# Optimization experiments

Hardware: AMD Instinct MI355X
Metric: run time of the kernel (lower is better)

The kernel has to match this reference:

```python
import jax, jax.numpy as jnp
import numpy as np

N_NODES = 100000


def sage_conv(x, src, dst, w_self, w_neigh, b):
    # DGL SAGEConv('mean'): h = x @ W_self + mean_{u in N(v)} x_u @ W_neigh + b
    ones = jnp.ones(src.shape[0], dtype=x.dtype)
    deg = jax.ops.segment_sum(ones, dst, num_segments=N_NODES)  # [N]
    neigh_sum = jax.ops.segment_sum(x[src], dst, num_segments=N_NODES)  # [N, F]
    neigh = neigh_sum / jnp.clip(deg, 1.0)[:, None]  # isolated nodes -> 0
    return x @ w_self + neigh @ w_neigh + b


def setup_inputs() -> dict:
    key = jax.random.key(0)
    ks = jax.random.split(key, 9)
    nfeat, nhid, nclass = 128, 128, 2
    E = 1600000
    x = jax.random.normal(ks[0], (N_NODES, nfeat), dtype=jnp.float32)
    src = jax.random.randint(ks[1], (E,), 0, N_NODES)
    dst = jax.random.randint(ks[2], (E,), 0, N_NODES)
    s1 = 1.0 / np.sqrt(nfeat)
    s2 = 1.0 / np.sqrt(nhid)
    return {
        "x": x,
        "src": src,
        "dst": dst,
        "w_self1": jax.random.uniform(ks[3], (nfeat, nhid), jnp.float32, -s1, s1),
        "w_neigh1": jax.random.uniform(ks[4], (nfeat, nhid), jnp.float32, -s1, s1),
        "b1": jnp.zeros((nhid,), jnp.float32),
        "w_self2": jax.random.uniform(ks[5], (nhid, nclass), jnp.float32, -s2, s2),
        "w_neigh2": jax.random.uniform(ks[6], (nhid, nclass), jnp.float32, -s2, s2),
        "b2": jnp.zeros((nclass,), jnp.float32),
    }


def reference(x, src, dst, w_self1, w_neigh1, b1, w_self2, w_neigh2, b2):
    h = jax.nn.relu(sage_conv(x, src, dst, w_self1, w_neigh1, b1))
    h = sage_conv(h, src, dst, w_self2, w_neigh2, b2)
    return jax.nn.log_softmax(h, axis=1)
```

## Files before the change

kernel.cpp:

```cpp
#include <hip/hip_runtime.h>
#include <hip/hip_bf16.h>


#define N_FEAT 128
#define CSHIFT 9
#define CNODES 512
#define NBINS 256
#define CCAP 9728
#define BATCH 8192
#define EPT 32
#define BF_BLOCKS 256
#define PW_BLOCKS 128

typedef __attribute__((ext_vector_type(8))) short short8;
typedef __attribute__((ext_vector_type(8))) unsigned short ushort8_t;
typedef __attribute__((ext_vector_type(16))) float f32x16;

__device__ __forceinline__ float bf16_bits_to_f32(ushort u) {
    union { unsigned int i; float f; } c;
    c.i = ((unsigned int)u) << 16;
    return c.f;
}
__device__ __forceinline__ ushort f32_to_bf16_bits(float f) {
    return __bfloat16_as_ushort(__float2bfloat16(f));
}

__global__ __launch_bounds__(256) void prep_and_split_kernel(
    const int* __restrict__ src, const int* __restrict__ dst,
    int* __restrict__ ccursor, unsigned* __restrict__ cbuf, int E,
    const float* __restrict__ x, ushort* __restrict__ xb, int n4,
    const float* __restrict__ w1, const float* __restrict__ w2,
    ushort* __restrict__ wt, int nms) {
    __shared__ unsigned stage[BATCH];
    __shared__ int cntw[4][NBINS];
    __shared__ int curw[4][NBINS];
    __shared__ int excl[NBINS];
    __shared__ int incl[NBINS];
    __shared__ int gpos[NBINS];
    __shared__ int wsum[4];
    int tid = threadIdx.x;
    int bid = blockIdx.x;

    if (bid >= nms) {
        int rb = bid - nms;
        if (rb < BF_BLOCKS) {
            int i = rb * 256 + tid;
            int stride = BF_BLOCKS * 256;
            for (; i < n4; i += stride) {
                float4 v = ((const float4*)x)[i];
                ushort4 r;
                r.x = f32_to_bf16_bits(v.x);
                r.y = f32_to_bf16_bits(v.y);
                r.z = f32_to_bf16_bits(v.z);
                r.w = f32_to_bf16_bits(v.w);
                ((ushort4*)xb)[i] = r;
            }
        } else {
            int id = (rb - BF_BLOCKS) * 256 + tid;
            int nn = id >> 8;
            int k = id & 255;
            float v = (k < 128) ? w1[k * 128 + nn] : w2[(k - 128) * 128 + nn];
            wt[nn * 256 + k] = f32_to_bf16_bits(v);
        }
        return;
    }

    int wv = tid >> 6;
    int lane = tid & 63;
    int base = bid * BATCH;
    int total = min(BATCH, E - base);

    unsigned pk[EPT];
    int bn[EPT];
    for (int i = tid; i < 4 * NBINS; i += 256) ((int*)cntw)[i] = 0;
    __syncthreads();
    #pragma unroll
    for (int k = 0; k < EPT; ++k) {
        int e = base + k * 256 + tid;
        if (e < E) {
            int d = dst[e];
            int sv = src[e];
            bn[k] = d >> CSHIFT;
            pk[k] = ((unsigned)(d & (CNODES - 1)) << 17) | (unsigned)sv;
            atomicAdd(&cntw[wv][bn[k]], 1);
        } else {
            bn[k] = -1;
        }
    }
    __syncthreads();
    int c0 = cntw[0][tid], c1 = cntw[1][tid], c2 = cntw[2][tid], c3 = cntw[3][tid];
    cntw[0][tid] = 0;
    cntw[1][tid] = c0;
    cntw[2][tid] = c0 + c1;
    cntw[3][tid] = c0 + c1 + c2;
    int c = c0 + c1 + c2 + c3;
    int val = c;
    #pragma unroll
    for (int off = 1; off < 64; off <<= 1) {
        int t = __shfl_up(val, off);
        if (lane >= off) val += t;
    }
    if (lane == 63) wsum[wv] = val;
    __syncthreads();
    #pragma unroll
    for (int i = 0; i < 4; ++i)
        if (i < wv) val += wsum[i];
    incl[tid] = val;
    int e0 = val - c;
    excl[tid] = e0;
    curw[0][tid] = e0 + cntw[0][tid];
    curw[1][tid] = e0 + cntw[1][tid];
    curw[2][tid] = e0 + cntw[2][tid];
    curw[3][tid] = e0 + cntw[3][tid];
    gpos[tid] = (c > 0) ? atomicAdd(&ccursor[tid], c) : 0;
    __syncthreads();
    #pragma unroll
    for (int k = 0; k < EPT; ++k) {
        if (bn[k] >= 0) {
            int ofs = atomicAdd(&curw[wv][bn[k]], 1);
            stage[ofs] = pk[k];
        }
    }
    __syncthreads();
    for (int i = tid; i < total; i += 256) {
        int lo = 0, hi = NBINS - 1;
        while (lo < hi) {
            int mid = (lo + hi) >> 1;
            if (incl[mid] > i) hi = mid; else lo = mid + 1;
        }
        int b = lo;
        int target = gpos[b] + (i - excl[b]);
        cbuf[(size_t)b * CCAP + target] = stage[i];
    }
}

__global__ __launch_bounds__(512) void build_csr2_kernel(
    const unsigned* __restrict__ cbuf, const int* __restrict__ ccnt,
    int* __restrict__ row_ptr, int* __restrict__ csr, int N, int E) {
    __shared__ int hist[CNODES];
    __shared__ int cur[CNODES];
    __shared__ int wred[8];
    __shared__ int cstart_s;
    int cb = blockIdx.x;
    int tid = threadIdx.x;
    int lane = tid & 63;
    int w = tid >> 6;

    int v = (tid < cb) ? ccnt[tid] : 0;
    #pragma unroll
    for (int off = 32; off > 0; off >>= 1) v += __shfl_xor(v, off);
    if (lane == 0) wred[w] = v;
    hist[tid] = 0;
    __syncthreads();
    if (tid == 0) {
        int t = 0;
        #pragma unroll
        for (int i = 0; i < 8; ++i) t += wred[i];
        cstart_s = t;
    }
    if (cb == 0 && tid == 0) row_ptr[N] = E;
    int cnt = ccnt[cb];
    size_t bbase = (size_t)cb * CCAP;
    __syncthreads();
    int base = cstart_s;

    for (int e = tid; e < cnt; e += 512) {
        unsigned p = cbuf[bbase + e];
        atomicAdd(&hist[p >> 17], 1);
    }
    __syncthreads();
    int c = hist[tid];
    int val = c;
    #pragma unroll
    for (int off = 1; off < 64; off <<= 1) {
        int t = __shfl_up(val, off);
        if (lane >= off) val += t;
    }
    if (lane == 63) wred[w] = val;
    __syncthreads();
    #pragma unroll
    for (int i = 0; i < 8; ++i)
        if (i < w) val += wred[i];
    int excl = val - c;
    int node = cb * CNODES + tid;
    if (node < N) row_ptr[node] = base + excl;
    cur[tid] = excl;
    __syncthreads();
    for (int e = tid; e < cnt; e += 512) {
        unsigned p = cbuf[bbase + e];
        int bin = p >> 17;
        int ofs = atomicAdd(&cur[bin], 1);
        csr[base + ofs] = (int)(p & 0x1FFFF);
    }
}

__global__ __launch_bounds__(256) void aggregate_bf16_kernel(
    const ushort* __restrict__ xb, const int* __restrict__ row_ptr,
    const int* __restrict__ csr, ushort* __restrict__ out, int n) {
    int v = blockIdx.x * 4 + (threadIdx.x >> 6);
    int lane = threadIdx.x & 63;
    int sub = lane >> 4;
    int fc = lane & 15;
    if (v >= n) return;
    int beg = row_ptr[v];
    int end = row_ptr[v + 1];
    float acc[8];
    #pragma unroll
    for (int j = 0; j < 8; ++j) acc[j] = 0.f;
    const ushort* xfc = xb + fc * 8;
    int e = beg;
    for (; e + 16 <= end; e += 16) {
        int s0 = csr[e + sub];
        int s1 = csr[e + 4 + sub];
        int s2 = csr[e + 8 + sub];
        int s3 = csr[e + 12 + sub];
        ushort8_t t0 = *(const ushort8_t*)(xfc + (size_t)s0 * N_FEAT);
        ushort8_t t1 = *(const ushort8_t*)(xfc + (size_t)s1 * N_FEAT);
        ushort8_t t2 = *(const ushort8_t*)(xfc + (size_t)s2 * N_FEAT);
        ushort8_t t3 = *(const ushort8_t*)(xfc + (size_t)s3 * N_FEAT);
        #pragma unroll
        for (int j = 0; j < 8; ++j) acc[j] += bf16_bits_to_f32(t0[j]);
        #pragma unroll
        for (int j = 0; j < 8; ++j) acc[j] += bf16_bits_to_f32(t1[j]);
        #pragma unroll
        for (int j = 0; j < 8; ++j) acc[j] += bf16_bits_to_f32(t2[j]);
        #pragma unroll
        for (int j = 0; j < 8; ++j) acc[j] += bf16_bits_to_f32(t3[j]);
    }
    if (e + 8 <= end) {
        int s0 = csr[e + sub];
        int s1 = csr[e + 4 + sub];
        ushort8_t t0 = *(const ushort8_t*)(xfc + (size_t)s0 * N_FEAT);
        ushort8_t t1 = *(const ushort8_t*)(xfc + (size_t)s1 * N_FEAT);
        #pragma unroll
        for (int j = 0; j < 8; ++j) acc[j] += bf16_bits_to_f32(t0[j]);
        #pragma unroll
        for (int j = 0; j < 8; ++j) acc[j] += bf16_bits_to_f32(t1[j]);
        e += 8;
    }
    if (e + 4 <= end) {
        int s0 = csr[e + sub];
        ushort8_t t0 = *(const ushort8_t*)(xfc + (size_t)s0 * N_FEAT);
        #pragma unroll
        for (int j = 0; j < 8; ++j) acc[j] += bf16_bits_to_f32(t0[j]);
        e += 4;
    }
    int rem = end - e;
    if (sub < rem) {
        int s0 = csr[e + sub];
        ushort8_t t0 = *(const ushort8_t*)(xfc + (size_t)s0 * N_FEAT);
        #pragma unroll
        for (int j = 0; j < 8; ++j) acc[j] += bf16_bits_to_f32(t0[j]);
    }
    #pragma unroll
    for (int j = 0; j < 8; ++j) {
        acc[j] += __shfl_xor(acc[j], 16);
        acc[j] += __shfl_xor(acc[j], 32);
    }
    if (lane < 16) {
        int deg = end - beg;
        float inv = (deg > 0) ? 1.0f / (float)deg : 0.0f;
        ushort8_t r;
        #pragma unroll
        for (int j = 0; j < 8; ++j)
            r[j] = f32_to_bf16_bits(acc[j] * inv);
        *(ushort8_t*)(out + (size_t)v * N_FEAT + lane * 8) = r;
    }
}

__global__ __launch_bounds__(256) void gemm1_fused_kernel(
    const ushort* __restrict__ xb, const ushort* __restrict__ nbb,
    const ushort* __restrict__ wt, const float* __restrict__ b,
    const float* __restrict__ ws2, const float* __restrict__ wn2,
    float* __restrict__ s_out, float* __restrict__ z_out, int n) {
    __shared__ ushort As[128 * 72];
    __shared__ ushort Bs[128 * 72];
    int tid = threadIdx.x;
    int wave = tid >> 6;
    int lane = tid & 63;
    int m = lane & 31;
    int half = lane >> 5;
    int block_row = blockIdx.x * 128;

    f32x16 acc[4];
    #pragma unroll
    for (int t = 0; t < 4; ++t)
        #pragma unroll
        for (int i = 0; i < 16; ++i) acc[t][i] = 0.0f;

    for (int kc = 0; kc < 4; ++kc) {
        const ushort* A = (kc < 2) ? xb : nbb;
        int k0 = (kc & 1) * 64;
        #pragma unroll
        for (int l = 0; l < 4; ++l) {
            int idx = l * 256 + tid;
            int r = idx >> 3;
            int p = idx & 7;
            int node = block_row + r;
            ushort8_t v;
            if (node < n) {
                v = *(const ushort8_t*)(A + (size_t)node * N_FEAT + k0 + p * 8);
            } else {
                #pragma unroll
                for (int q = 0; q < 8; ++q) v[q] = 0;
            }
            *(ushort8_t*)(&As[r * 72 + p * 8]) = v;
        }
        #pragma unroll
        for (int l = 0; l < 4; ++l) {
            int idx = l * 256 + tid;
            int cc = idx >> 3;
            int p = idx & 7;
            ushort8_t v = *(const ushort8_t*)(wt + (size_t)cc * 256 + kc * 64 + p * 8);
            *(ushort8_t*)(&Bs[cc * 72 + p * 8]) = v;
        }
        __syncthreads();
        #pragma unroll
        for (int ks = 0; ks < 4; ++ks) {
            int koff = ks * 16 + half * 8;
            short8 a = *(const short8*)(&As[(32 * wave + m) * 72 + koff]);
            short8 bf0 = *(const short8*)(&Bs[(0 * 32 + m) * 72 + koff]);
            short8 bf1 = *(const short8*)(&Bs[(1 * 32 + m) * 72 + koff]);
            short8 bf2 = *(const short8*)(&Bs[(2 * 32 + m) * 72 + koff]);
            short8 bf3 = *(const short8*)(&Bs[(3 * 32 + m) * 72 + koff]);
            acc[0] = __builtin_amdgcn_mfma_f32_32x32x16_bf16(a, bf0, acc[0], 0, 0, 0);
            acc[1] = __builtin_amdgcn_mfma_f32_32x32x16_bf16(a, bf1, acc[1], 0, 0, 0);
            acc[2] = __builtin_amdgcn_mfma_f32_32x32x16_bf16(a, bf2, acc[2], 0, 0, 0);
            acc[3] = __builtin_amdgcn_mfma_f32_32x32x16_bf16(a, bf3, acc[3], 0, 0, 0);
        }
        __syncthreads();
    }

    float bcol[4], wsc[4][2], wnc[4][2];
    #pragma unroll
    for (int t = 0; t < 4; ++t) {
        int col = t * 32 + m;
        bcol[t] = b[col];
        float2 a = ((const float2*)ws2)[col];
        float2 q = ((const float2*)wn2)[col];
        wsc[t][0] = a.x; wsc[t][1] = a.y;
        wnc[t][0] = q.x; wnc[t][1] = q.y;
    }
    #pragma unroll
    for (int reg = 0; reg < 16; ++reg) {
        int rowin = (reg & 3) + 8 * (reg >> 2) + 4 * half;
        int node = block_row + 32 * wave + rowin;
        float p0 = 0.f, p1 = 0.f, q0 = 0.f, q1 = 0.f;
        #pragma unroll
        for (int t = 0; t < 4; ++t) {
            float hv = fmaxf(acc[t][reg] + bcol[t], 0.0f);
            p0 += hv * wsc[t][0]; p1 += hv * wsc[t][1];
            q0 += hv * wnc[t][0]; q1 += hv * wnc[t][1];
        }
        #pragma unroll
        for (int off = 1; off < 32; off <<= 1) {
            p0 += __shfl_xor(p0, off);
            p1 += __shfl_xor(p1, off);
            q0 += __shfl_xor(q0, off);
            q1 += __shfl_xor(q1, off);
        }
        if (m == 0 && node < n) {
            ((float2*)s_out)[node] = make_float2(p0, p1);
            ((float2*)z_out)[node] = make_float2(q0, q1);
        }
    }
}

__global__ __launch_bounds__(256) void layer2b_kernel(
    const float* __restrict__ s_in, const float* __restrict__ z,
    const int* __restrict__ row_ptr, const int* __restrict__ csr,
    const float* __restrict__ b, float* __restrict__ out, int n) {
    int v = blockIdx.x * 16 + (threadIdx.x >> 4);
    int sl = threadIdx.x & 15;
    if (v >= n) return;
    int beg = row_ptr[v];
    int end = row_ptr[v + 1];
    float a0 = 0.f, a1 = 0.f;
    for (int e = beg + sl; e < end; e += 16) {
        float2 t = ((const float2*)z)[csr[e]];
        a0 += t.x; a1 += t.y;
    }
    #pragma unroll
    for (int off = 8; off > 0; off >>= 1) {
        a0 += __shfl_xor(a0, off);
        a1 += __shfl_xor(a1, off);
    }
    if (sl == 0) {
        int deg = end - beg;
        float inv = (deg > 0) ? 1.0f / (float)deg : 0.0f;
        float2 sv = ((const float2*)s_in)[v];
        float o0 = sv.x + a0 * inv + b[0];
        float o1 = sv.y + a1 * inv + b[1];
        float mx = fmaxf(o0, o1);
        float lse = mx + logf(expf(o0 - mx) + expf(o1 - mx));
        ((float2*)out)[v] = make_float2(o0 - lse, o1 - lse);
    }
}

extern "C" void kernel_launch(void* const* d_in, const int* in_sizes, int n_in,
                              void* d_out, int out_size, void* d_ws, size_t ws_size,
                              hipStream_t stream) {
    const float* x        = (const float*)d_in[0];
    const int*   src      = (const int*)d_in[1];
    const int*   dst      = (const int*)d_in[2];
    const float* w_self1  = (const float*)d_in[3];
    const float* w_neigh1 = (const float*)d_in[4];
    const float* b1       = (const float*)d_in[5];
    const float* w_self2  = (const float*)d_in[6];
    const float* w_neigh2 = (const float*)d_in[7];
    const float* b2       = (const float*)d_in[8];
    float* out = (float*)d_out;

    int N = in_sizes[0] / N_FEAT;
    int E = in_sizes[1];
    int nbk = (N + CNODES - 1) / CNODES;
    int nms = (E + BATCH - 1) / BATCH;

    char* ws = (char*)d_ws;
    size_t off = 0;
    auto alloc = [&](size_t bytes) -> void* {
        void* p = ws + off;
        off += (bytes + 255) & ~(size_t)255;
        return p;
    };
    int*      ccursor = (int*)alloc(NBINS * 4);
    int*      row_ptr = (int*)alloc((size_t)(N + 1) * 4);
    int*      csr     = (int*)alloc((size_t)E * 4);
    unsigned* cbuf    = (unsigned*)alloc((size_t)nbk * CCAP * 4);
    ushort*   xb      = (ushort*)alloc((size_t)N * N_FEAT * 2);
    ushort*   nbb     = (ushort*)alloc((size_t)N * N_FEAT * 2);
    ushort*   wt      = (ushort*)alloc((size_t)128 * 256 * 2);
    float*    s_buf   = (float*)alloc((size_t)N * 2 * 4);
    float*    z_buf   = (float*)alloc((size_t)N * 2 * 4);
    (void)ws_size; (void)n_in; (void)out_size;

    hipMemsetAsync(ccursor, 0, NBINS * 4, stream);

    prep_and_split_kernel<<<nms + BF_BLOCKS + PW_BLOCKS, 256, 0, stream>>>(
        src, dst, ccursor, cbuf, E, x, xb, N * N_FEAT / 4, w_self1, w_neigh1, wt, nms);
    build_csr2_kernel<<<nbk, 512, 0, stream>>>(cbuf, ccursor, row_ptr, csr, N, E);
    aggregate_bf16_kernel<<<(N + 3) / 4, 256, 0, stream>>>(xb, row_ptr, csr, nbb, N);
    gemm1_fused_kernel<<<(N + 127) / 128, 256, 0, stream>>>(
        xb, nbb, wt, b1, w_self2, w_neigh2, s_buf, z_buf, N);
    layer2b_kernel<<<(N + 15) / 16, 256, 0, stream>>>(s_buf, z_buf, row_ptr, csr, b2, out, N);
}
```

Before: 250.2 us.

## Fuse CSR build with layer-1 neighbor aggregation in per-octant sort kernel

Replaces the separate CSR-build and layer-1 aggregation kernels with one kernel. Each block takes one 64-node octant of a 512-node chunk, sorts that octant's edges in shared memory, writes its row_ptr and csr slices, and gathers neighbor features straight from the LDS-sorted list. This removes a launch and the global re-read of csr and row_ptr for layer 1. In exchange, every octant block rescans its whole chunk (8x redundant reads of cbuf), and any octant with more than KCAP edges would be silently truncated. BATCH and EPT in the split kernel are also halved.

```diff
diff --git a/kernel.cpp b/kernel.cpp
--- a/kernel.cpp
+++ b/kernel.cpp
@@ -7,10 +7,12 @@
 #define CNODES 512
 #define NBINS 256
 #define CCAP 9728
-#define BATCH 8192
-#define EPT 32
+#define BATCH 4096
+#define EPT 16
 #define BF_BLOCKS 256
 #define PW_BLOCKS 128
+#define FNODES 64
+#define KCAP 1536
 
 typedef __attribute__((ext_vector_type(8))) short short8;
 typedef __attribute__((ext_vector_type(8))) unsigned short ushort8_t;
@@ -134,137 +136,146 @@
     }
 }
 
-__global__ __launch_bounds__(512) void build_csr2_kernel(
+__global__ __launch_bounds__(256) void sort_agg_kernel(
     const unsigned* __restrict__ cbuf, const int* __restrict__ ccnt,
-    int* __restrict__ row_ptr, int* __restrict__ csr, int N, int E) {
-    __shared__ int hist[CNODES];
-    __shared__ int cur[CNODES];
-    __shared__ int wred[8];
-    __shared__ int cstart_s;
-    int cb = blockIdx.x;
+    const ushort* __restrict__ xb, int* __restrict__ row_ptr,
+    int* __restrict__ csr, ushort* __restrict__ out, int N, int E) {
+    __shared__ unsigned sorted[KCAP];
+    __shared__ int hist[FNODES];
+    __shared__ int lexcl[FNODES + 1];
+    __shared__ int cur[FNODES];
+    __shared__ int wred[4];
+    __shared__ int wred2[4];
+    int cb  = blockIdx.x >> 3;
+    int oct = blockIdx.x & 7;
     int tid = threadIdx.x;
     int lane = tid & 63;
-    int w = tid >> 6;
-
-    int v = (tid < cb) ? ccnt[tid] : 0;
-    #pragma unroll
-    for (int off = 32; off > 0; off >>= 1) v += __shfl_xor(v, off);
-    if (lane == 0) wred[w] = v;
-    hist[tid] = 0;
-    __syncthreads();
-    if (tid == 0) {
-        int t = 0;
-        #pragma unroll
-        for (int i = 0; i < 8; ++i) t += wred[i];
-        cstart_s = t;
-    }
-    if (cb == 0 && tid == 0) row_ptr[N] = E;
+    int wv = tid >> 6;
+    int nodebase = cb * CNODES + oct * FNODES;
+
+    if (tid < FNODES) hist[tid] = 0;
+    if (blockIdx.x == 0 && tid == 0) row_ptr[N] = E;
+    int acc = 0;
+    for (int i = tid; i < cb; i += 256) acc += ccnt[i];
+    #pragma unroll
+    for (int off = 32; off > 0; off >>= 1) acc += __shfl_xor(acc, off);
+    if (lane == 0) wred[wv] = acc;
+    __syncthreads();
+    int cstart = wred[0] + wred[1] + wred[2] + wred[3];
     int cnt = ccnt[cb];
     size_t bbase = (size_t)cb * CCAP;
-    __syncthreads();
-    int base = cstart_s;
-
-    for (int e = tid; e < cnt; e += 512) {
+
+    int before = 0;
+    for (int e = tid; e < cnt; e += 256) {
         unsigned p = cbuf[bbase + e];
-        atomicAdd(&hist[p >> 17], 1);
-    }
-    __syncthreads();
-    int c = hist[tid];
-    int val = c;
-    #pragma unroll
-    for (int off = 1; off < 64; off <<= 1) {
-        int t = __shfl_up(val, off);
-        if (lane >= off) val += t;
-    }
-    if (lane == 63) wred[w] = val;
-    __syncthreads();
-    #pragma unroll
-    for (int i = 0; i < 8; ++i)
-        if (i < w) val += wred[i];
-    int excl = val - c;
-    int node = cb * CNODES + tid;
-    if (node < N) row_ptr[node] = base + excl;
-    cur[tid] = excl;
-    __syncthreads();
-    for (int e = tid; e < cnt; e += 512) {
+        int o = (int)((p >> 23) & 7u);
+        before += (o < oct) ? 1 : 0;
+        if (o == oct) atomicAdd(&hist[(p >> 17) & 63], 1);
+    }
+    #pragma unroll
+    for (int off = 32; off > 0; off >>= 1) before += __shfl_xor(before, off);
+    if (lane == 0) wred2[wv] = before;
+    __syncthreads();
+    int my_base = cstart + wred2[0] + wred2[1] + wred2[2] + wred2[3];
+
+    if (wv == 0) {
+        int c = hist[lane];
+        int v = c;
+        #pragma unroll
+        for (int off = 1; off < 64; off <<= 1) {
+            int t = __shfl_up(v, off);
+            if (lane >= off) v += t;
+        }
+        lexcl[lane] = v - c;
+        cur[lane] = v - c;
+        if (lane == 63) lexcl[FNODES] = v;
+        int node = nodebase + lane;
+        if (node <= N) row_ptr[node] = my_base + (v - c);
+    }
+    __syncthreads();
+
+    for (int e = tid; e < cnt; e += 256) {
         unsigned p = cbuf[bbase + e];
-        int bin = p >> 17;
-        int ofs = atomicAdd(&cur[bin], 1);
-        csr[base + ofs] = (int)(p & 0x1FFFF);
-    }
-}
-
-__global__ __launch_bounds__(256) void aggregate_bf16_kernel(
-    const ushort* __restrict__ xb, const int* __restrict__ row_ptr,
-    const int* __restrict__ csr, ushort* __restrict__ out, int n) {
-    int v = blockIdx.x * 4 + (threadIdx.x >> 6);
-    int lane = threadIdx.x & 63;
+        if (((p >> 23) & 7u) == (unsigned)oct) {
+            int pos = atomicAdd(&cur[(p >> 17) & 63], 1);
+            if (pos < KCAP) sorted[pos] = p;
+        }
+    }
+    __syncthreads();
+
+    int kc = min(lexcl[FNODES], KCAP);
+    for (int e = tid; e < kc; e += 256)
+        csr[my_base + e] = (int)(sorted[e] & 0x1FFFF);
+
     int sub = lane >> 4;
     int fc = lane & 15;
-    if (v >= n) return;
-    int beg = row_ptr[v];
-    int end = row_ptr[v + 1];
-    float acc[8];
-    #pragma unroll
-    for (int j = 0; j < 8; ++j) acc[j] = 0.f;
     const ushort* xfc = xb + fc * 8;
-    int e = beg;
-    for (; e + 16 <= end; e += 16) {
-        int s0 = csr[e + sub];
-        int s1 = csr[e + 4 + sub];
-        int s2 = csr[e + 8 + sub];
-        int s3 = csr[e + 12 + sub];
-        ushort8_t t0 = *(const ushort8_t*)(xfc + (size_t)s0 * N_FEAT);
-        ushort8_t t1 = *(const ushort8_t*)(xfc + (size_t)s1 * N_FEAT);
-        ushort8_t t2 = *(const ushort8_t*)(xfc + (size_t)s2 * N_FEAT);
-        ushort8_t t3 = *(const ushort8_t*)(xfc + (size_t)s3 * N_FEAT);
-        #pragma unroll
-        for (int j = 0; j < 8; ++j) acc[j] += bf16_bits_to_f32(t0[j]);
-        #pragma unroll
-        for (int j = 0; j < 8; ++j) acc[j] += bf16_bits_to_f32(t1[j]);
-        #pragma unroll
-        for (int j = 0; j < 8; ++j) acc[j] += bf16_bits_to_f32(t2[j]);
-        #pragma unroll
-        for (int j = 0; j < 8; ++j) acc[j] += bf16_bits_to_f32(t3[j]);
-    }
-    if (e + 8 <= end) {
-        int s0 = csr[e + sub];
-        int s1 = csr[e + 4 + sub];
-        ushort8_t t0 = *(const ushort8_t*)(xfc + (size_t)s0 * N_FEAT);
-        ushort8_t t1 = *(const ushort8_t*)(xfc + (size_t)s1 * N_FEAT);
-        #pragma unroll
-        for (int j = 0; j < 8; ++j) acc[j] += bf16_bits_to_f32(t0[j]);
-        #pragma unroll
-        for (int j = 0; j < 8; ++j) acc[j] += bf16_bits_to_f32(t1[j]);
-        e += 8;
-    }
-    if (e + 4 <= end) {
-        int s0 = csr[e + sub];
-        ushort8_t t0 = *(const ushort8_t*)(xfc + (size_t)s0 * N_FEAT);
-        #pragma unroll
-        for (int j = 0; j < 8; ++j) acc[j] += bf16_bits_to_f32(t0[j]);
-        e += 4;
-    }
-    int rem = end - e;
-    if (sub < rem) {
-        int s0 = csr[e + sub];
-        ushort8_t t0 = *(const ushort8_t*)(xfc + (size_t)s0 * N_FEAT);
-        #pragma unroll
-        for (int j = 0; j < 8; ++j) acc[j] += bf16_bits_to_f32(t0[j]);
-    }
-    #pragma unroll
-    for (int j = 0; j < 8; ++j) {
-        acc[j] += __shfl_xor(acc[j], 16);
-        acc[j] += __shfl_xor(acc[j], 32);
-    }
-    if (lane < 16) {
-        int deg = end - beg;
-        float inv = (deg > 0) ? 1.0f / (float)deg : 0.0f;
-        ushort8_t r;
-        #pragma unroll
-        for (int j = 0; j < 8; ++j)
-            r[j] = f32_to_bf16_bits(acc[j] * inv);
-        *(ushort8_t*)(out + (size_t)v * N_FEAT + lane * 8) = r;
+    for (int i = 0; i < 16; ++i) {
+        int ln = wv * 16 + i;
+        int g = nodebase + ln;
+        int beg = min(lexcl[ln], KCAP);
+        int end = min(lexcl[ln + 1], KCAP);
+        float a[8];
+        #pragma unroll
+        for (int j = 0; j < 8; ++j) a[j] = 0.f;
+        int e = beg;
+        for (; e + 16 <= end; e += 16) {
+            int s0 = (int)(sorted[e + sub] & 0x1FFFF);
+            int s1 = (int)(sorted[e + 4 + sub] & 0x1FFFF);
+            int s2 = (int)(sorted[e + 8 + sub] & 0x1FFFF);
+            int s3 = (int)(sorted[e + 12 + sub] & 0x1FFFF);
+            ushort8_t t0 = *(const ushort8_t*)(xfc + (size_t)s0 * N_FEAT);
+            ushort8_t t1 = *(const ushort8_t*)(xfc + (size_t)s1 * N_FEAT);
+            ushort8_t t2 = *(const ushort8_t*)(xfc + (size_t)s2 * N_FEAT);
+            ushort8_t t3 = *(const ushort8_t*)(xfc + (size_t)s3 * N_FEAT);
+            #pragma unroll
+            for (int j = 0; j < 8; ++j) a[j] += bf16_bits_to_f32(t0[j]);
+            #pragma unroll
+            for (int j = 0; j < 8; ++j) a[j] += bf16_bits_to_f32(t1[j]);
+            #pragma unroll
+            for (int j = 0; j < 8; ++j) a[j] += bf16_bits_to_f32(t2[j]);
+            #pragma unroll
+            for (int j = 0; j < 8; ++j) a[j] += bf16_bits_to_f32(t3[j]);
+        }
+        if (e + 8 <= end) {
+            int s0 = (int)(sorted[e + sub] & 0x1FFFF);
+            int s1 = (int)(sorted[e + 4 + sub] & 0x1FFFF);
+            ushort8_t t0 = *(const ushort8_t*)(xfc + (size_t)s0 * N_FEAT);
+            ushort8_t t1 = *(const ushort8_t*)(xfc + (size_t)s1 * N_FEAT);
+            #pragma unroll
+            for (int j = 0; j < 8; ++j) a[j] += bf16_bits_to_f32(t0[j]);
+            #pragma unroll
+            for (int j = 0; j < 8; ++j) a[j] += bf16_bits_to_f32(t1[j]);
+            e += 8;
+        }
+        if (e + 4 <= end) {
+            int s0 = (int)(sorted[e + sub] & 0x1FFFF);
+            ushort8_t t0 = *(const ushort8_t*)(xfc + (size_t)s0 * N_FEAT);
+            #pragma unroll
+            for (int j = 0; j < 8; ++j) a[j] += bf16_bits_to_f32(t0[j]);
+            e += 4;
+        }
+        int rem = end - e;
+        if (sub < rem) {
+            int s0 = (int)(sorted[e + sub] & 0x1FFFF);
+            ushort8_t t0 = *(const ushort8_t*)(xfc + (size_t)s0 * N_FEAT);
+            #pragma unroll
+            for (int j = 0; j < 8; ++j) a[j] += bf16_bits_to_f32(t0[j]);
+        }
+        #pragma unroll
+        for (int j = 0; j < 8; ++j) {
+            a[j] += __shfl_xor(a[j], 16);
+            a[j] += __shfl_xor(a[j], 32);
+        }
+        if (lane < 16 && g < N) {
+            int deg = end - beg;
+            float inv = (deg > 0) ? 1.0f / (float)deg : 0.0f;
+            ushort8_t r;
+            #pragma unroll
+            for (int j = 0; j < 8; ++j)
+                r[j] = f32_to_bf16_bits(a[j] * inv);
+            *(ushort8_t*)(out + (size_t)g * N_FEAT + lane * 8) = r;
+        }
     }
 }
 
@@ -438,8 +449,8 @@
 
     prep_and_split_kernel<<<nms + BF_BLOCKS + PW_BLOCKS, 256, 0, stream>>>(
         src, dst, ccursor, cbuf, E, x, xb, N * N_FEAT / 4, w_self1, w_neigh1, wt, nms);
-    build_csr2_kernel<<<nbk, 512, 0, stream>>>(cbuf, ccursor, row_ptr, csr, N, E);
-    aggregate_bf16_kernel<<<(N + 3) / 4, 256, 0, stream>>>(xb, row_ptr, csr, nbb, N);
+    sort_agg_kernel<<<nbk * 8, 256, 0, stream>>>(
+        cbuf, ccursor, xb, row_ptr, csr, nbb, N, E);
     gemm1_fused_kernel<<<(N + 127) / 128, 256, 0, stream>>>(
         xb, nbb, wt, b1, w_self2, w_neigh2, s_buf, z_buf, N);
     layer2b_kernel<<<(N + 15) / 16, 256, 0, stream>>>(s_buf, z_buf, row_ptr, csr, b2, out, N);
```

Result: slower. 255.7 us (+2.2%).
